# Kernel tuning notes

Hardware: AMD Instinct MI355X
Metric: run time of the kernel (lower is better)

The kernel has to match this reference:

```python
import jax, jax.numpy as jnp
import numpy as np

B, S, D, C, K, V = 128, 512, 300, 300, 3, 30000  # batch, seq, embed=hidden, capsule, categories, vocab
PAD_INDEX = 0
SQUASH_EPS = 1e-8
MASK_NEG = -1e9


def squash(x, axis=-1):
    # v * (|v|^2 / (1+|v|^2)) / |v|
    sq = jnp.sum(x * x, axis=axis, keepdims=True)
    return (sq / (1.0 + sq)) * x / jnp.sqrt(sq + SQUASH_EPS)


def setup_inputs() -> dict:
    key = jax.random.key(0)
    ks = jax.random.split(key, 11)
    return {
        "sentence": jax.random.randint(ks[0], (B, S), 0, V),
        "aspect": jax.random.randint(ks[1], (B,), 0, V),
        "category_alpha": jax.random.uniform(ks[2], (B, S), dtype=jnp.float32),
        "embed": jax.random.normal(ks[3], (V, D), dtype=jnp.float32) * 0.02,
        "W_s": jax.random.normal(ks[4], (D, C), dtype=jnp.float32) * 0.02,
        "b_s": jnp.zeros((C,), dtype=jnp.float32),
        "W_a": jax.random.normal(ks[5], (D, C), dtype=jnp.float32) * 0.02,
        "b_a": jnp.zeros((C,), dtype=jnp.float32),
        "W_att": jax.random.normal(ks[6], (C, C), dtype=jnp.float32) * 0.02,
        "guide_capsule": jax.random.normal(ks[7], (K, C), dtype=jnp.float32) * 0.02,
        "guide_weight": jax.random.normal(ks[8], (C, C), dtype=jnp.float32) * 0.02,
        "scale": jnp.asarray(5.0, dtype=jnp.float32),
    }


def reference(sentence, aspect, category_alpha, embed, W_s, b_s, W_a, b_a,
              W_att, guide_capsule, guide_weight, scale):
    mask = sentence != PAD_INDEX                      # [B,S]
    emb = embed[sentence]                             # [B,S,D]
    asp = embed[aspect]                               # [B,D]

    # element_wise_mul (vectorized): per-token alpha weighting
    caml = emb * category_alpha[..., None]            # [B,S,D]
    cavl = jnp.sum(caml, axis=1)                      # [B,D] (unused in non-Cav path)
    del cavl

    # _sentence_encode stand-in (abstract in source): alpha-weighted embeddings
    sent_enc = caml                                   # [B,S,hidden=D]

    primary = squash(sent_enc @ W_s + b_s)            # [B,S,C]
    aspect_capsule = squash(asp @ W_a + b_a)          # [B,C]

    # bilinear attention weights with padding mask, softmax over sequence
    scores = jnp.einsum('bsc,cd,bd->bs', primary, W_att, aspect_capsule)
    scores = jnp.where(mask, scores, MASK_NEG)
    norm_weight = jax.nn.softmax(scores, axis=-1)     # [B,S]

    # capsule-guided routing
    guide = squash(guide_capsule)                     # [K,C]
    gm = jnp.einsum('bsc,cd,kd->bsk', primary, guide_weight, guide)
    gm = jax.nn.softmax(gm, axis=-1) * norm_weight[..., None] * scale
    category_capsule = squash(jnp.einsum('bsk,bsc->bkc', gm, primary))  # [B,K,C]

    return jnp.sqrt(jnp.sum(category_capsule * category_capsule, axis=-1))  # [B,K]
```

## Files before the change

### kernel.cpp

```cpp
#include <hip/hip_runtime.h>

#define NV 30000
#define NB 128
#define NS 512
#define ND 300
#define NC 300
#define CP 304
#define KP 320
#define EP 320
#define ETW 136
#define MASK_NEG -1e9f
#define SQ_EPS 1e-8f

typedef __attribute__((ext_vector_type(4))) float f32x4;
typedef __attribute__((ext_vector_type(8))) __bf16 bf16x8;

__device__ __forceinline__ unsigned short f2bf(float x){
  unsigned int u = __float_as_uint(x);
  u += 0x7FFFu + ((u >> 16) & 1u);
  return (unsigned short)(u >> 16);
}
__device__ __forceinline__ float bf2f(unsigned short h){
  return __uint_as_float(((unsigned int)h) << 16);
}

__device__ __forceinline__ float bsum512(float v, float* red, int tid){
  red[tid] = v; __syncthreads();
  float s = 0.f;
  if (tid < 64){
    s = red[tid]+red[tid+64]+red[tid+128]+red[tid+192]
      + red[tid+256]+red[tid+320]+red[tid+384]+red[tid+448];
    #pragma unroll
    for (int off = 32; off > 0; off >>= 1) s += __shfl_xor(s, off);
    if (tid == 0) red[0] = s;
  }
  __syncthreads();
  s = red[0];
  __syncthreads();
  return s;
}

__device__ __forceinline__ float bmax512(float v, float* red, int tid){
  red[tid] = v; __syncthreads();
  float s = MASK_NEG;
  if (tid < 64){
    s = red[tid];
    #pragma unroll
    for (int o = 64; o < 512; o += 64) s = fmaxf(s, red[tid+o]);
    #pragma unroll
    for (int off = 32; off > 0; off >>= 1) s = fmaxf(s, __shfl_xor(s, off));
    if (tid == 0) red[0] = s;
  }
  __syncthreads();
  s = red[0];
  __syncthreads();
  return s;
}

__global__ __launch_bounds__(512) void kprep(
    const float* __restrict__ Ws, const float* __restrict__ Watt,
    const float* __restrict__ Gw, const float* __restrict__ bs,
    const float* __restrict__ gcap, const int* __restrict__ aspect,
    const float* __restrict__ embed, const float* __restrict__ Wa,
    const float* __restrict__ ba,
    unsigned short* __restrict__ wt, float* __restrict__ bsp,
    float* __restrict__ tbuf, float* __restrict__ gbuf)
{
  int bid = blockIdx.x, tid = threadIdx.x;
  int lane = tid & 63, w = tid >> 6;
  __shared__ float sh[64*65];
  float* aspL = sh;
  float* capL = sh + 320;
  float* red  = sh + 640;

  if (bid < 25) {
    float (*t)[65] = (float(*)[65])sh;
    int kt = bid / 5, nt = bid - kt*5;
    #pragma unroll
    for (int i = 0; i < 8; i++){
      int idx = i*512 + tid;
      int r = idx >> 6, c = idx & 63;
      int gk = kt*64 + r, gn = nt*64 + c;
      t[r][c] = (gk < ND && gn < NC) ? Ws[gk*NC + gn] : 0.f;
    }
    __syncthreads();
    #pragma unroll
    for (int i = 0; i < 8; i++){
      int idx = i*512 + tid;
      int n = idx >> 6, k = idx & 63;
      wt[(nt*64 + n)*KP + kt*64 + k] = f2bf(t[k][n]);
    }
  } else if (bid == 25) {
    if (tid < 320) bsp[tid] = (tid < NC) ? bs[tid] : 0.f;
  } else if (bid < 154) {
    int b = bid - 26;
    int a = aspect[b];
    if (tid < 320) aspL[tid] = (tid < ND) ? embed[(size_t)a*ND + tid] : 0.f;
    __syncthreads();
    int c = tid;
    float p0=0.f,p1=0.f,p2=0.f,p3=0.f,p4=0.f,p5=0.f;
    if (c < NC){
      for (int d = 0; d < 300; d += 6){
        p0 += Wa[(d+0)*NC + c]*aspL[d+0];
        p1 += Wa[(d+1)*NC + c]*aspL[d+1];
        p2 += Wa[(d+2)*NC + c]*aspL[d+2];
        p3 += Wa[(d+3)*NC + c]*aspL[d+3];
        p4 += Wa[(d+4)*NC + c]*aspL[d+4];
        p5 += Wa[(d+5)*NC + c]*aspL[d+5];
      }
    }
    float z = (c < NC) ? (ba[c] + ((p0+p1)+(p2+p3)+(p4+p5))) : 0.f;
    float sq = bsum512((c < NC) ? z*z : 0.f, red, tid);
    float ssv = (sq/(1.f+sq))/sqrtf(sq + SQ_EPS);
    if (tid < 320) capL[tid] = (c < NC) ? z*ssv : 0.f;
    __syncthreads();
    for (int cc = w; cc < NC; cc += 8){
      const float* wr = Watt + (size_t)cc*NC;
      float acc = 0.f;
      #pragma unroll
      for (int j = 0; j < 5; j++){
        int d = j*64 + lane;
        float wv = (d < ND) ? wr[d] : 0.f;
        acc += wv*capL[d];
      }
      #pragma unroll
      for (int off = 32; off > 0; off >>= 1) acc += __shfl_xor(acc, off);
      if (lane == 0) tbuf[(size_t)b*CP + cc] = acc;
    }
    if (tid < 4) tbuf[(size_t)b*CP + NC + tid] = 0.f;
  } else {
    int k = bid - 154;
    if (tid < 320) aspL[tid] = (tid < NC) ? gcap[k*NC + tid] : 0.f;
    __syncthreads();
    float g = (tid < 320) ? aspL[tid] : 0.f;
    float sq = bsum512((tid < NC) ? g*g : 0.f, red, tid);
    float ssv = (sq/(1.f+sq))/sqrtf(sq + SQ_EPS);
    if (tid < 320) capL[tid] = g*ssv;
    __syncthreads();
    for (int cc = w; cc < NC; cc += 8){
      const float* wr = Gw + (size_t)cc*NC;
      float acc = 0.f;
      #pragma unroll
      for (int j = 0; j < 5; j++){
        int d = j*64 + lane;
        float wv = (d < ND) ? wr[d] : 0.f;
        acc += wv*capL[d];
      }
      #pragma unroll
      for (int off = 32; off > 0; off >>= 1) acc += __shfl_xor(acc, off);
      if (lane == 0) gbuf[(size_t)k*CP + cc] = acc;
    }
    if (tid < 4) gbuf[(size_t)k*CP + NC + tid] = 0.f;
  }
}

#define BM 64
#define BKT 64
#define LDK 72
__global__ __launch_bounds__(512) void k1_gemm(
    const float* __restrict__ embed, const unsigned short* __restrict__ wt,
    unsigned short* __restrict__ E, float* __restrict__ EtT)
{
  __shared__ unsigned short lds_a[BM*LDK];
  __shared__ unsigned short lds_b[KP*LDK];
  __shared__ float e2part[4][BM];
  int tid = threadIdx.x;
  int lane = tid & 63, wid = tid >> 6;
  int wrow = wid >> 2, wcol = wid & 3;
  int rowbase = blockIdx.x * BM;
  f32x4 acc[2][5];
  f32x4 zero = {0.f,0.f,0.f,0.f};
  #pragma unroll
  for (int m = 0; m < 2; m++)
    #pragma unroll
    for (int n = 0; n < 5; n++) acc[m][n] = zero;

  for (int k0 = 0; k0 < KP; k0 += BKT){
    #pragma unroll
    for (int r = 0; r < 2; r++){
      int id = r*512 + tid;
      int row = id >> 4, k4 = (id & 15) << 2;
      int gk = k0 + k4, grow = rowbase + row;
      float4 v = {0.f,0.f,0.f,0.f};
      if (grow < NV && gk < ND) v = *(const float4*)(embed + (size_t)grow*ND + gk);
      unsigned int lo = (unsigned int)f2bf(v.x) | ((unsigned int)f2bf(v.y) << 16);
      unsigned int hi = (unsigned int)f2bf(v.z) | ((unsigned int)f2bf(v.w) << 16);
      uint2 pk; pk.x = lo; pk.y = hi;
      *(uint2*)(lds_a + row*LDK + k4) = pk;
    }
    #pragma unroll
    for (int r = 0; r < 5; r++){
      int id = r*512 + tid;
      int n = id >> 3, koff = (id & 7) << 3;
      uint4 v = *(const uint4*)(wt + n*KP + k0 + koff);
      *(uint4*)(lds_b + n*LDK + koff) = v;
    }
    __syncthreads();
    #pragma unroll
    for (int kk = 0; kk < BKT; kk += 32){
      bf16x8 af[2], bfr[5];
      int kidx = kk + (lane >> 4)*8;
      int arow = wrow*32 + (lane & 15);
      int brow = wcol*80 + (lane & 15);
      #pragma unroll
      for (int m = 0; m < 2; m++) af[m] = *(const bf16x8*)(lds_a + (arow + m*16)*LDK + kidx);
      #pragma unroll
      for (int n = 0; n < 5; n++) bfr[n] = *(const bf16x8*)(lds_b + (brow + n*16)*LDK + kidx);
      #pragma unroll
      for (int m = 0; m < 2; m++)
        #pragma unroll
        for (int n = 0; n < 5; n++)
          acc[m][n] = __builtin_amdgcn_mfma_f32_16x16x32_bf16(af[m], bfr[n], acc[m][n], 0, 0, 0);
    }
    __syncthreads();
  }
  int colb = wcol*80 + (lane & 15);
  int rowb = rowbase + wrow*32 + ((lane >> 4) << 2);
  #pragma unroll
  for (int m = 0; m < 2; m++)
    #pragma unroll
    for (int n = 0; n < 5; n++)
      #pragma unroll
      for (int j = 0; j < 4; j++){
        int row = rowb + m*16 + j;
        int col = colb + n*16;
        if (row < NV) E[(size_t)row*EP + col] = f2bf(acc[m][n][j]);
      }
  #pragma unroll
  for (int m = 0; m < 2; m++)
    #pragma unroll
    for (int j = 0; j < 4; j++){
      float p = 0.f;
      #pragma unroll
      for (int n = 0; n < 5; n++){ float t = acc[m][n][j]; p += t*t; }
      #pragma unroll
      for (int off = 1; off < 16; off <<= 1) p += __shfl_xor(p, off);
      if ((lane & 15) == 0)
        e2part[wcol][wrow*32 + m*16 + ((lane >> 4) << 2) + j] = p;
    }
  __syncthreads();
  if (tid < BM){
    int grow = rowbase + tid;
    if (grow < NV){
      float s = e2part[0][tid] + e2part[1][tid] + e2part[2][tid] + e2part[3][tid];
      EtT[(size_t)grow*ETW + 132] = s;
    }
  }
}

#define BM2 128
#define BN2 160
#define LDK2 72
__global__ __launch_bounds__(512) void k1b_gemm(
    const unsigned short* __restrict__ E, const float* __restrict__ tbuf,
    const float* __restrict__ gbuf, const float* __restrict__ bsp,
    float* __restrict__ EtT)
{
  __shared__ unsigned short la[BM2*LDK2];
  __shared__ unsigned short lb[BN2*LDK2];
  int tid = threadIdx.x;
  int lane = tid & 63, wid = tid >> 6;
  int wrow = wid >> 1, wcol = wid & 1;
  int rowbase = blockIdx.x * BM2;
  f32x4 acc[2][5];
  f32x4 zero = {0.f,0.f,0.f,0.f};
  #pragma unroll
  for (int m = 0; m < 2; m++)
    #pragma unroll
    for (int n = 0; n < 5; n++) acc[m][n] = zero;

  for (int k0 = 0; k0 < EP; k0 += 64){
    #pragma unroll
    for (int r = 0; r < 2; r++){
      int id = r*512 + tid;
      int row = id >> 3, koff = (id & 7) << 3;
      int grow = rowbase + row, gk = k0 + koff;
      uint4 v = {0u,0u,0u,0u};
      if (grow < NV){
        v = *(const uint4*)(E + (size_t)grow*EP + gk);
      } else if (grow == NV){
        float4 f0 = *(const float4*)(bsp + gk);
        float4 f1 = *(const float4*)(bsp + gk + 4);
        v.x = (unsigned int)f2bf(f0.x) | ((unsigned int)f2bf(f0.y) << 16);
        v.y = (unsigned int)f2bf(f0.z) | ((unsigned int)f2bf(f0.w) << 16);
        v.z = (unsigned int)f2bf(f1.x) | ((unsigned int)f2bf(f1.y) << 16);
        v.w = (unsigned int)f2bf(f1.z) | ((unsigned int)f2bf(f1.w) << 16);
      }
      *(uint4*)(la + row*LDK2 + koff) = v;
    }
    #pragma unroll
    for (int r = 0; r < 5; r++){
      int id = r*512 + tid;
      int n = id >> 4, k4 = (id & 15) << 2;
      int gk = k0 + k4;
      float4 f = {0.f,0.f,0.f,0.f};
      if (gk < CP){
        if (n < 128)       f = *(const float4*)(tbuf + (size_t)n*CP + gk);
        else if (n < 131)  f = *(const float4*)(gbuf + (size_t)(n-128)*CP + gk);
        else if (n == 131) f = *(const float4*)(bsp + gk);
      }
      uint2 pk;
      pk.x = (unsigned int)f2bf(f.x) | ((unsigned int)f2bf(f.y) << 16);
      pk.y = (unsigned int)f2bf(f.z) | ((unsigned int)f2bf(f.w) << 16);
      *(uint2*)(lb + n*LDK2 + k4) = pk;
    }
    __syncthreads();
    #pragma unroll
    for (int kk = 0; kk < 64; kk += 32){
      bf16x8 af[2], bfr[5];
      int kidx = kk + (lane >> 4)*8;
      int arow = wrow*32 + (lane & 15);
      int brow = wcol*80 + (lane & 15);
      #pragma unroll
      for (int m = 0; m < 2; m++) af[m] = *(const bf16x8*)(la + (arow + m*16)*LDK2 + kidx);
      #pragma unroll
      for (int n = 0; n < 5; n++) bfr[n] = *(const bf16x8*)(lb + (brow + n*16)*LDK2 + kidx);
      #pragma unroll
      for (int m = 0; m < 2; m++)
        #pragma unroll
        for (int n = 0; n < 5; n++)
          acc[m][n] = __builtin_amdgcn_mfma_f32_16x16x32_bf16(af[m], bfr[n], acc[m][n], 0, 0, 0);
    }
    __syncthreads();
  }
  int colb = wcol*80 + (lane & 15);
  int rowb = rowbase + wrow*32 + ((lane >> 4) << 2);
  #pragma unroll
  for (int m = 0; m < 2; m++)
    #pragma unroll
    for (int n = 0; n < 5; n++)
      #pragma unroll
      for (int j = 0; j < 4; j++){
        int row = rowb + m*16 + j;
        int col = colb + n*16;
        if (row <= NV && col < 132) EtT[(size_t)row*ETW + col] = acc[m][n][j];
      }
}

__global__ __launch_bounds__(512) void k45(
    const int* __restrict__ sentence, const float* __restrict__ alpha,
    const float* __restrict__ scale_p, const unsigned short* __restrict__ E,
    const float* __restrict__ EtT, const float* __restrict__ bsp,
    float* __restrict__ out)
{
  int b = blockIdx.x, tid = threadIdx.x;
  int lane = tid & 63, w = tid >> 6;
  __shared__ float red[512];
  __shared__ float cfs[NS*3];
  __shared__ int toksh[NS];
  __shared__ float cap8[8][3][CP];
  __shared__ float vall[3*CP];

  int idx = (b << 9) + tid;
  int tok = sentence[idx];
  float al = alpha[idx];
  toksh[tid] = tok;
  const float* er = EtT + (size_t)tok*ETW;
  float e2v = er[132];
  float et  = er[b];
  float g0  = er[128], g1 = er[129], g2 = er[130];
  float ebs = er[131];
  const float* br = EtT + (size_t)NV*ETW;
  float bst = br[b];
  float bsg0 = br[128], bsg1 = br[129], bsg2 = br[130], bs2 = br[131];

  float sq  = al*al*e2v + 2.f*al*ebs + bs2;
  float ssv = (sq/(1.f+sq))/sqrtf(sq + SQ_EPS);
  float scv = (tok != 0) ? ssv*(al*et + bst) : MASK_NEG;
  float u0 = ssv*(al*g0 + bsg0);
  float u1 = ssv*(al*g1 + bsg1);
  float u2 = ssv*(al*g2 + bsg2);

  float m = bmax512(scv, red, tid);
  float e = expf(scv - m);
  float Z = bsum512(e, red, tid);
  float nw = e / Z;
  float mk = fmaxf(u0, fmaxf(u1, u2));
  float e0 = expf(u0-mk), e1 = expf(u1-mk), e2 = expf(u2-mk);
  float wf = nw * scale_p[0] / (e0+e1+e2);
  float w0 = e0*wf, w1 = e1*wf, w2 = e2*wf;
  float ca = ssv * al;
  cfs[tid*3+0] = w0*ca; cfs[tid*3+1] = w1*ca; cfs[tid*3+2] = w2*ca;
  float sb0 = bsum512(w0*ssv, red, tid);
  float sb1 = bsum512(w1*ssv, red, tid);
  float sb2 = bsum512(w2*ssv, red, tid);
  __syncthreads();

  f32x4 A0 = {0.f,0.f,0.f,0.f}, A1 = A0, A2 = A0, R0 = A0, R1 = A0, R2 = A0;
  int c0 = lane << 2;
  int c1 = 256 + (lane << 2);
  bool rem = lane < 12;
  int base = w << 6;
  #pragma unroll 4
  for (int i = 0; i < 64; i++){
    int s = base + i;
    int t = toksh[s];
    const unsigned short* erow = E + (size_t)t*EP;
    uint2 ev = *(const uint2*)(erow + c0);
    float cf0 = cfs[s*3+0], cf1 = cfs[s*3+1], cf2 = cfs[s*3+2];
    f32x4 y;
    y[0] = bf2f((unsigned short)(ev.x & 0xffffu));
    y[1] = bf2f((unsigned short)(ev.x >> 16));
    y[2] = bf2f((unsigned short)(ev.y & 0xffffu));
    y[3] = bf2f((unsigned short)(ev.y >> 16));
    A0 += cf0*y; A1 += cf1*y; A2 += cf2*y;
    if (rem){
      uint2 ev2 = *(const uint2*)(erow + c1);
      f32x4 yr;
      yr[0] = bf2f((unsigned short)(ev2.x & 0xffffu));
      yr[1] = bf2f((unsigned short)(ev2.x >> 16));
      yr[2] = bf2f((unsigned short)(ev2.y & 0xffffu));
      yr[3] = bf2f((unsigned short)(ev2.y >> 16));
      R0 += cf0*yr; R1 += cf1*yr; R2 += cf2*yr;
    }
  }
  *(f32x4*)&cap8[w][0][c0] = A0;
  *(f32x4*)&cap8[w][1][c0] = A1;
  *(f32x4*)&cap8[w][2][c0] = A2;
  if (rem){
    *(f32x4*)&cap8[w][0][c1] = R0;
    *(f32x4*)&cap8[w][1][c1] = R1;
    *(f32x4*)&cap8[w][2][c1] = R2;
  }
  __syncthreads();
  float sbk[3] = {sb0, sb1, sb2};
  for (int p = tid; p < 3*CP; p += 512){
    int k = p / CP, c = p - k*CP;
    float v = sbk[k]*bsp[c];
    #pragma unroll
    for (int w8 = 0; w8 < 8; w8++) v += cap8[w8][k][c];
    vall[p] = v;
  }
  __syncthreads();
  #pragma unroll
  for (int k = 0; k < 3; k++){
    float x = 0.f;
    if (tid < CP){ float t = vall[k*CP + tid]; x = t*t; }
    float s = bsum512(x, red, tid);
    if (tid == 0){
      out[b*3 + k] = (s/(1.f+s))*sqrtf(s)/sqrtf(s + SQ_EPS);
    }
  }
}

extern "C" void kernel_launch(void* const* d_in, const int* in_sizes, int n_in,
                              void* d_out, int out_size, void* d_ws, size_t ws_size,
                              hipStream_t stream)
{
  (void)in_sizes; (void)n_in; (void)out_size; (void)ws_size;
  const int*   sentence = (const int*)d_in[0];
  const int*   aspect   = (const int*)d_in[1];
  const float* alpha    = (const float*)d_in[2];
  const float* embed    = (const float*)d_in[3];
  const float* Ws       = (const float*)d_in[4];
  const float* bs       = (const float*)d_in[5];
  const float* Wa       = (const float*)d_in[6];
  const float* ba       = (const float*)d_in[7];
  const float* Watt     = (const float*)d_in[8];
  const float* gcap     = (const float*)d_in[9];
  const float* gw       = (const float*)d_in[10];
  const float* scale    = (const float*)d_in[11];
  float* out = (float*)d_out;

  char* w = (char*)d_ws;
  auto alloc = [&](size_t bytes)->char*{
    char* p = w; w += (bytes + 255) & ~(size_t)255; return p;
  };
  unsigned short* WT  = (unsigned short*)alloc((size_t)KP*KP*2);
  unsigned short* E   = (unsigned short*)alloc((size_t)NV*EP*2);
  float* ETT = (float*)alloc((size_t)(NV+1)*ETW*4);
  float* BSP = (float*)alloc(320*4);
  float* TBF = (float*)alloc((size_t)NB*CP*4);
  float* GBF = (float*)alloc(3*CP*4);

  kprep<<<157, 512, 0, stream>>>(Ws, Watt, gw, bs, gcap, aspect, embed, Wa, ba,
                                 WT, BSP, TBF, GBF);
  k1_gemm<<<(NV + BM - 1)/BM, 512, 0, stream>>>(embed, WT, E, ETT);
  k1b_gemm<<<(NV + 1 + BM2 - 1)/BM2, 512, 0, stream>>>(E, TBF, GBF, BSP, ETT);
  k45<<<NB, 512, 0, stream>>>(sentence, alpha, scale, E, ETT, BSP, out);
}
```

Baseline: 106.5 us.

## Fuse second projection GEMM into the embedding GEMM via LDS-resident tile

Merges k1_gemm and k1b_gemm. Each block keeps its bf16 projected embedding tile in LDS and immediately multiplies it by a prebuilt bf16 matrix of aspect, guide and bias vectors (BMT, built in kprep), so E no longer has to be re-read from global memory. An extra block handles the bias row. The per-token score table is split into a 128-wide array plus an 8-wide side array, and E's pitch shrinks to 304. This removes one launch and the E round trip, but the second GEMM reads its B operand directly from global memory without staging, and the tile's LDS reuse adds some pressure.

Result: slower. 112.3 us (+5.5%).

```diff
diff --git a/kernel.cpp b/kernel.cpp
--- a/kernel.cpp
+++ b/kernel.cpp
@@ -7,8 +7,7 @@
 #define NC 300
 #define CP 304
 #define KP 320
-#define EP 320
-#define ETW 136
+#define EP 304
 #define MASK_NEG -1e9f
 #define SQ_EPS 1e-8f
 
@@ -64,7 +63,7 @@
     const float* __restrict__ embed, const float* __restrict__ Wa,
     const float* __restrict__ ba,
     unsigned short* __restrict__ wt, float* __restrict__ bsp,
-    float* __restrict__ tbuf, float* __restrict__ gbuf)
+    unsigned short* __restrict__ BMT)
 {
   int bid = blockIdx.x, tid = threadIdx.x;
   int lane = tid & 63, w = tid >> 6;
@@ -91,7 +90,13 @@
       wt[(nt*64 + n)*KP + kt*64 + k] = f2bf(t[k][n]);
     }
   } else if (bid == 25) {
-    if (tid < 320) bsp[tid] = (tid < NC) ? bs[tid] : 0.f;
+    float bv = 0.f;
+    if (tid < 320){
+      bv = (tid < NC) ? bs[tid] : 0.f;
+      bsp[tid] = bv;
+      BMT[131*KP + tid] = f2bf(bv);
+    }
+    for (int i = tid; i < 28*KP; i += 512) BMT[132*KP + i] = 0;
   } else if (bid < 154) {
     int b = bid - 26;
     int a = aspect[b];
@@ -125,9 +130,9 @@
       }
       #pragma unroll
       for (int off = 32; off > 0; off >>= 1) acc += __shfl_xor(acc, off);
-      if (lane == 0) tbuf[(size_t)b*CP + cc] = acc;
-    }
-    if (tid < 4) tbuf[(size_t)b*CP + NC + tid] = 0.f;
+      if (lane == 0) BMT[(size_t)b*KP + cc] = f2bf(acc);
+    }
+    if (tid < 20) BMT[(size_t)b*KP + 300 + tid] = 0;
   } else {
     int k = bid - 154;
     if (tid < 320) aspL[tid] = (tid < NC) ? gcap[k*NC + tid] : 0.f;
@@ -148,200 +153,155 @@
       }
       #pragma unroll
       for (int off = 32; off > 0; off >>= 1) acc += __shfl_xor(acc, off);
-      if (lane == 0) gbuf[(size_t)k*CP + cc] = acc;
-    }
-    if (tid < 4) gbuf[(size_t)k*CP + NC + tid] = 0.f;
+      if (lane == 0) BMT[(size_t)(128+k)*KP + cc] = f2bf(acc);
+    }
+    if (tid < 20) BMT[(size_t)(128+k)*KP + 300 + tid] = 0;
   }
 }
 
 #define BM 64
 #define BKT 64
 #define LDK 72
-__global__ __launch_bounds__(512) void k1_gemm(
+#define LDE 328
+__global__ __launch_bounds__(512) void k1f(
     const float* __restrict__ embed, const unsigned short* __restrict__ wt,
-    unsigned short* __restrict__ E, float* __restrict__ EtT)
+    const unsigned short* __restrict__ BMT, const float* __restrict__ bsp,
+    unsigned short* __restrict__ E, float* __restrict__ EtT,
+    float* __restrict__ ETS)
 {
   __shared__ unsigned short lds_a[BM*LDK];
   __shared__ unsigned short lds_b[KP*LDK];
   __shared__ float e2part[4][BM];
   int tid = threadIdx.x;
   int lane = tid & 63, wid = tid >> 6;
-  int wrow = wid >> 2, wcol = wid & 3;
-  int rowbase = blockIdx.x * BM;
-  f32x4 acc[2][5];
-  f32x4 zero = {0.f,0.f,0.f,0.f};
-  #pragma unroll
-  for (int m = 0; m < 2; m++)
-    #pragma unroll
-    for (int n = 0; n < 5; n++) acc[m][n] = zero;
-
-  for (int k0 = 0; k0 < KP; k0 += BKT){
-    #pragma unroll
-    for (int r = 0; r < 2; r++){
-      int id = r*512 + tid;
-      int row = id >> 4, k4 = (id & 15) << 2;
-      int gk = k0 + k4, grow = rowbase + row;
-      float4 v = {0.f,0.f,0.f,0.f};
-      if (grow < NV && gk < ND) v = *(const float4*)(embed + (size_t)grow*ND + gk);
-      unsigned int lo = (unsigned int)f2bf(v.x) | ((unsigned int)f2bf(v.y) << 16);
-      unsigned int hi = (unsigned int)f2bf(v.z) | ((unsigned int)f2bf(v.w) << 16);
-      uint2 pk; pk.x = lo; pk.y = hi;
-      *(uint2*)(lds_a + row*LDK + k4) = pk;
-    }
-    #pragma unroll
-    for (int r = 0; r < 5; r++){
-      int id = r*512 + tid;
-      int n = id >> 3, koff = (id & 7) << 3;
-      uint4 v = *(const uint4*)(wt + n*KP + k0 + koff);
-      *(uint4*)(lds_b + n*LDK + koff) = v;
-    }
-    __syncthreads();
-    #pragma unroll
-    for (int kk = 0; kk < BKT; kk += 32){
-      bf16x8 af[2], bfr[5];
-      int kidx = kk + (lane >> 4)*8;
-      int arow = wrow*32 + (lane & 15);
-      int brow = wcol*80 + (lane & 15);
-      #pragma unroll
-      for (int m = 0; m < 2; m++) af[m] = *(const bf16x8*)(lds_a + (arow + m*16)*LDK + kidx);
-      #pragma unroll
-      for (int n = 0; n < 5; n++) bfr[n] = *(const bf16x8*)(lds_b + (brow + n*16)*LDK + kidx);
-      #pragma unroll
-      for (int m = 0; m < 2; m++)
-        #pragma unroll
-        for (int n = 0; n < 5; n++)
-          acc[m][n] = __builtin_amdgcn_mfma_f32_16x16x32_bf16(af[m], bfr[n], acc[m][n], 0, 0, 0);
-    }
-    __syncthreads();
-  }
-  int colb = wcol*80 + (lane & 15);
-  int rowb = rowbase + wrow*32 + ((lane >> 4) << 2);
-  #pragma unroll
-  for (int m = 0; m < 2; m++)
-    #pragma unroll
-    for (int n = 0; n < 5; n++)
+  int bid = blockIdx.x;
+  bool special = (bid == (NV + BM - 1)/BM);
+  int rowbase = special ? NV : bid * BM;
+  unsigned short* et = lds_b;
+
+  if (!special){
+    int wrow = wid >> 2, wcol = wid & 3;
+    f32x4 acc[2][5];
+    f32x4 zero = {0.f,0.f,0.f,0.f};
+    #pragma unroll
+    for (int m = 0; m < 2; m++)
+      #pragma unroll
+      for (int n = 0; n < 5; n++) acc[m][n] = zero;
+
+    for (int k0 = 0; k0 < KP; k0 += BKT){
+      #pragma unroll
+      for (int r = 0; r < 2; r++){
+        int id = r*512 + tid;
+        int row = id >> 4, k4 = (id & 15) << 2;
+        int gk = k0 + k4, grow = rowbase + row;
+        float4 v = {0.f,0.f,0.f,0.f};
+        if (grow < NV && gk < ND) v = *(const float4*)(embed + (size_t)grow*ND + gk);
+        unsigned int lo = (unsigned int)f2bf(v.x) | ((unsigned int)f2bf(v.y) << 16);
+        unsigned int hi = (unsigned int)f2bf(v.z) | ((unsigned int)f2bf(v.w) << 16);
+        uint2 pk; pk.x = lo; pk.y = hi;
+        *(uint2*)(lds_a + row*LDK + k4) = pk;
+      }
+      #pragma unroll
+      for (int r = 0; r < 5; r++){
+        int id = r*512 + tid;
+        int n = id >> 3, koff = (id & 7) << 3;
+        uint4 v = *(const uint4*)(wt + n*KP + k0 + koff);
+        *(uint4*)(lds_b + n*LDK + koff) = v;
+      }
+      __syncthreads();
+      #pragma unroll
+      for (int kk = 0; kk < BKT; kk += 32){
+        bf16x8 af[2], bfr[5];
+        int kidx = kk + (lane >> 4)*8;
+        int arow = wrow*32 + (lane & 15);
+        int brow = wcol*80 + (lane & 15);
+        #pragma unroll
+        for (int m = 0; m < 2; m++) af[m] = *(const bf16x8*)(lds_a + (arow + m*16)*LDK + kidx);
+        #pragma unroll
+        for (int n = 0; n < 5; n++) bfr[n] = *(const bf16x8*)(lds_b + (brow + n*16)*LDK + kidx);
+        #pragma unroll
+        for (int m = 0; m < 2; m++)
+          #pragma unroll
+          for (int n = 0; n < 5; n++)
+            acc[m][n] = __builtin_amdgcn_mfma_f32_16x16x32_bf16(af[m], bfr[n], acc[m][n], 0, 0, 0);
+      }
+      __syncthreads();
+    }
+    int colb = wcol*80 + (lane & 15);
+    int rowb0 = wrow*32 + ((lane >> 4) << 2);
+    #pragma unroll
+    for (int m = 0; m < 2; m++)
+      #pragma unroll
+      for (int n = 0; n < 5; n++)
+        #pragma unroll
+        for (int j = 0; j < 4; j++){
+          int rloc = rowb0 + m*16 + j;
+          int row = rowbase + rloc;
+          int col = colb + n*16;
+          unsigned short h = f2bf(acc[m][n][j]);
+          if (row < NV && col < EP) E[(size_t)row*EP + col] = h;
+          et[rloc*LDE + col] = h;
+        }
+    #pragma unroll
+    for (int m = 0; m < 2; m++)
       #pragma unroll
       for (int j = 0; j < 4; j++){
-        int row = rowb + m*16 + j;
-        int col = colb + n*16;
-        if (row < NV) E[(size_t)row*EP + col] = f2bf(acc[m][n][j]);
-      }
-  #pragma unroll
-  for (int m = 0; m < 2; m++)
-    #pragma unroll
-    for (int j = 0; j < 4; j++){
-      float p = 0.f;
-      #pragma unroll
-      for (int n = 0; n < 5; n++){ float t = acc[m][n][j]; p += t*t; }
-      #pragma unroll
-      for (int off = 1; off < 16; off <<= 1) p += __shfl_xor(p, off);
-      if ((lane & 15) == 0)
-        e2part[wcol][wrow*32 + m*16 + ((lane >> 4) << 2) + j] = p;
-    }
-  __syncthreads();
-  if (tid < BM){
+        float p = 0.f;
+        #pragma unroll
+        for (int n = 0; n < 5; n++){ float t = acc[m][n][j]; p += t*t; }
+        #pragma unroll
+        for (int off = 1; off < 16; off <<= 1) p += __shfl_xor(p, off);
+        if ((lane & 15) == 0)
+          e2part[wcol][rowb0 + m*16 + j] = p;
+      }
+  } else {
+    for (int i = tid; i < 64*LDE; i += 512) et[i] = 0;
+    if (tid < 320) et[tid] = f2bf(bsp[tid]);
+  }
+  __syncthreads();
+  if (!special && tid < BM){
     int grow = rowbase + tid;
     if (grow < NV){
       float s = e2part[0][tid] + e2part[1][tid] + e2part[2][tid] + e2part[3][tid];
-      EtT[(size_t)grow*ETW + 132] = s;
-    }
-  }
-}
-
-#define BM2 128
-#define BN2 160
-#define LDK2 72
-__global__ __launch_bounds__(512) void k1b_gemm(
-    const unsigned short* __restrict__ E, const float* __restrict__ tbuf,
-    const float* __restrict__ gbuf, const float* __restrict__ bsp,
-    float* __restrict__ EtT)
-{
-  __shared__ unsigned short la[BM2*LDK2];
-  __shared__ unsigned short lb[BN2*LDK2];
-  int tid = threadIdx.x;
-  int lane = tid & 63, wid = tid >> 6;
-  int wrow = wid >> 1, wcol = wid & 1;
-  int rowbase = blockIdx.x * BM2;
-  f32x4 acc[2][5];
-  f32x4 zero = {0.f,0.f,0.f,0.f};
+      ETS[(size_t)grow*8 + 4] = s;
+    }
+  }
+  int wr2 = wid >> 1, wc2 = wid & 1;
+  f32x4 acc2[5];
+  f32x4 z2 = {0.f,0.f,0.f,0.f};
   #pragma unroll
-  for (int m = 0; m < 2; m++)
-    #pragma unroll
-    for (int n = 0; n < 5; n++) acc[m][n] = zero;
-
-  for (int k0 = 0; k0 < EP; k0 += 64){
-    #pragma unroll
-    for (int r = 0; r < 2; r++){
-      int id = r*512 + tid;
-      int row = id >> 3, koff = (id & 7) << 3;
-      int grow = rowbase + row, gk = k0 + koff;
-      uint4 v = {0u,0u,0u,0u};
-      if (grow < NV){
-        v = *(const uint4*)(E + (size_t)grow*EP + gk);
-      } else if (grow == NV){
-        float4 f0 = *(const float4*)(bsp + gk);
-        float4 f1 = *(const float4*)(bsp + gk + 4);
-        v.x = (unsigned int)f2bf(f0.x) | ((unsigned int)f2bf(f0.y) << 16);
-        v.y = (unsigned int)f2bf(f0.z) | ((unsigned int)f2bf(f0.w) << 16);
-        v.z = (unsigned int)f2bf(f1.x) | ((unsigned int)f2bf(f1.y) << 16);
-        v.w = (unsigned int)f2bf(f1.z) | ((unsigned int)f2bf(f1.w) << 16);
-      }
-      *(uint4*)(la + row*LDK2 + koff) = v;
-    }
-    #pragma unroll
-    for (int r = 0; r < 5; r++){
-      int id = r*512 + tid;
-      int n = id >> 4, k4 = (id & 15) << 2;
-      int gk = k0 + k4;
-      float4 f = {0.f,0.f,0.f,0.f};
-      if (gk < CP){
-        if (n < 128)       f = *(const float4*)(tbuf + (size_t)n*CP + gk);
-        else if (n < 131)  f = *(const float4*)(gbuf + (size_t)(n-128)*CP + gk);
-        else if (n == 131) f = *(const float4*)(bsp + gk);
-      }
-      uint2 pk;
-      pk.x = (unsigned int)f2bf(f.x) | ((unsigned int)f2bf(f.y) << 16);
-      pk.y = (unsigned int)f2bf(f.z) | ((unsigned int)f2bf(f.w) << 16);
-      *(uint2*)(lb + n*LDK2 + k4) = pk;
-    }
-    __syncthreads();
-    #pragma unroll
-    for (int kk = 0; kk < 64; kk += 32){
-      bf16x8 af[2], bfr[5];
-      int kidx = kk + (lane >> 4)*8;
-      int arow = wrow*32 + (lane & 15);
-      int brow = wcol*80 + (lane & 15);
-      #pragma unroll
-      for (int m = 0; m < 2; m++) af[m] = *(const bf16x8*)(la + (arow + m*16)*LDK2 + kidx);
-      #pragma unroll
-      for (int n = 0; n < 5; n++) bfr[n] = *(const bf16x8*)(lb + (brow + n*16)*LDK2 + kidx);
-      #pragma unroll
-      for (int m = 0; m < 2; m++)
-        #pragma unroll
-        for (int n = 0; n < 5; n++)
-          acc[m][n] = __builtin_amdgcn_mfma_f32_16x16x32_bf16(af[m], bfr[n], acc[m][n], 0, 0, 0);
-    }
-    __syncthreads();
-  }
-  int colb = wcol*80 + (lane & 15);
-  int rowb = rowbase + wrow*32 + ((lane >> 4) << 2);
+  for (int n = 0; n < 5; n++) acc2[n] = z2;
+  #pragma unroll 2
+  for (int kk = 0; kk < KP; kk += 32){
+    int kidx = kk + (lane >> 4)*8;
+    bf16x8 a2 = *(const bf16x8*)(et + (wr2*16 + (lane & 15))*LDE + kidx);
+    #pragma unroll
+    for (int n = 0; n < 5; n++){
+      bf16x8 b2 = *(const bf16x8*)(BMT + (size_t)(wc2*80 + n*16 + (lane & 15))*KP + kidx);
+      acc2[n] = __builtin_amdgcn_mfma_f32_16x16x32_bf16(a2, b2, acc2[n], 0, 0, 0);
+    }
+  }
+  int colb2 = wc2*80 + (lane & 15);
+  int rowb2 = rowbase + wr2*16 + ((lane >> 4) << 2);
+  int rlim = special ? (NV + 1) : NV;
   #pragma unroll
-  for (int m = 0; m < 2; m++)
-    #pragma unroll
-    for (int n = 0; n < 5; n++)
-      #pragma unroll
-      for (int j = 0; j < 4; j++){
-        int row = rowb + m*16 + j;
-        int col = colb + n*16;
-        if (row <= NV && col < 132) EtT[(size_t)row*ETW + col] = acc[m][n][j];
-      }
+  for (int n = 0; n < 5; n++)
+    #pragma unroll
+    for (int j = 0; j < 4; j++){
+      int row = rowb2 + j;
+      int col = colb2 + n*16;
+      if (row < rlim){
+        if (col < 128)      EtT[(size_t)row*128 + col] = acc2[n][j];
+        else if (col < 132) ETS[(size_t)row*8 + (col - 128)] = acc2[n][j];
+      }
+    }
 }
 
 __global__ __launch_bounds__(512) void k45(
     const int* __restrict__ sentence, const float* __restrict__ alpha,
     const float* __restrict__ scale_p, const unsigned short* __restrict__ E,
-    const float* __restrict__ EtT, const float* __restrict__ bsp,
-    float* __restrict__ out)
+    const float* __restrict__ EtT, const float* __restrict__ ETS,
+    const float* __restrict__ bsp, float* __restrict__ out)
 {
   int b = blockIdx.x, tid = threadIdx.x;
   int lane = tid & 63, w = tid >> 6;
@@ -355,21 +315,18 @@
   int tok = sentence[idx];
   float al = alpha[idx];
   toksh[tid] = tok;
-  const float* er = EtT + (size_t)tok*ETW;
-  float e2v = er[132];
-  float et  = er[b];
-  float g0  = er[128], g1 = er[129], g2 = er[130];
-  float ebs = er[131];
-  const float* br = EtT + (size_t)NV*ETW;
-  float bst = br[b];
-  float bsg0 = br[128], bsg1 = br[129], bsg2 = br[130], bs2 = br[131];
-
-  float sq  = al*al*e2v + 2.f*al*ebs + bs2;
+  float et  = EtT[(size_t)tok*128 + b];
+  float4 eg = *(const float4*)(ETS + (size_t)tok*8);
+  float e2v = ETS[(size_t)tok*8 + 4];
+  float bst = EtT[(size_t)NV*128 + b];
+  float4 brs = *(const float4*)(ETS + (size_t)NV*8);
+
+  float sq  = al*al*e2v + 2.f*al*eg.w + brs.w;
   float ssv = (sq/(1.f+sq))/sqrtf(sq + SQ_EPS);
   float scv = (tok != 0) ? ssv*(al*et + bst) : MASK_NEG;
-  float u0 = ssv*(al*g0 + bsg0);
-  float u1 = ssv*(al*g1 + bsg1);
-  float u2 = ssv*(al*g2 + bsg2);
+  float u0 = ssv*(al*eg.x + brs.x);
+  float u1 = ssv*(al*eg.y + brs.y);
+  float u2 = ssv*(al*eg.z + brs.z);
 
   float m = bmax512(scv, red, tid);
   float e = expf(scv - m);
@@ -468,14 +425,13 @@
   };
   unsigned short* WT  = (unsigned short*)alloc((size_t)KP*KP*2);
   unsigned short* E   = (unsigned short*)alloc((size_t)NV*EP*2);
-  float* ETT = (float*)alloc((size_t)(NV+1)*ETW*4);
+  float* ETT = (float*)alloc((size_t)(NV+1)*128*4);
+  float* ETS = (float*)alloc((size_t)(NV+1)*8*4);
   float* BSP = (float*)alloc(320*4);
-  float* TBF = (float*)alloc((size_t)NB*CP*4);
-  float* GBF = (float*)alloc(3*CP*4);
+  unsigned short* BMT = (unsigned short*)alloc((size_t)160*KP*2);
 
   kprep<<<157, 512, 0, stream>>>(Ws, Watt, gw, bs, gcap, aspect, embed, Wa, ba,
-                                 WT, BSP, TBF, GBF);
-  k1_gemm<<<(NV + BM - 1)/BM, 512, 0, stream>>>(embed, WT, E, ETT);
-  k1b_gemm<<<(NV + 1 + BM2 - 1)/BM2, 512, 0, stream>>>(E, TBF, GBF, BSP, ETT);
-  k45<<<NB, 512, 0, stream>>>(sentence, alpha, scale, E, ETT, BSP, out);
-}
+                                 WT, BSP, BMT);
+  k1f<<<(NV + BM - 1)/BM + 1, 512, 0, stream>>>(embed, WT, BMT, BSP, E, ETT, ETS);
+  k45<<<NB, 512, 0, stream>>>(sentence, alpha, scale, E, ETT, ETS, BSP, out);
+}
```
